# Kernel optimization log

Hardware: AMD Instinct MI355X
Metric: run time of the kernel (lower is better)

The kernel has to match this reference:

```python
import jax, jax.numpy as jnp
import numpy as np

B, S, D = 8, 2048, 64
NEG = -1e9


def setup_inputs() -> dict:
    key = jax.random.key(0)
    kq, kk, kv = jax.random.split(key, 3)
    return {
        "queries": jax.random.normal(kq, (B, S, D), dtype=jnp.float32),
        "keys": jax.random.normal(kk, (B, S, D), dtype=jnp.float32),
        "values": jax.random.normal(kv, (B, S, D), dtype=jnp.float32),
        "mask_q": jnp.ones((B, S), dtype=jnp.float32),
        "mask_k": jnp.ones((B, S), dtype=jnp.float32),
        "mask_v": jnp.ones((B, S), dtype=jnp.float32),
    }


def reference(queries, keys, values, mask_q, mask_k, mask_v):
    # scaled QK^T: [B, Sq, Sk]
    scaler = jnp.sqrt(jnp.asarray(queries.shape[-1], dtype=queries.dtype))
    scores = jnp.einsum("bqd,bkd->bqk", queries, keys) / scaler
    # additive padding mask from outer product of query/key masks
    padding_mask = mask_q[:, :, None] * mask_k[:, None, :]  # [B, Sq, Sk]
    scores = scores + (1.0 - padding_mask) * NEG
    attention_weights = jax.nn.softmax(scores, axis=-1)
    # mask values then weighted sum
    values = values * mask_v[:, :, None]
    output = jnp.einsum("bqk,bkd->bqd", attention_weights, values)
    return output
```

## Files before the change

kernel.cpp:

```cpp
#include <hip/hip_runtime.h>
#include <hip/hip_bf16.h>
#include <math.h>

#define BATCH 8
#define SEQ   2048
#define DIM   64
#define NEGC  (-1e9f)

typedef short short8  __attribute__((ext_vector_type(8)));
typedef float f32x4   __attribute__((ext_vector_type(4)));
typedef float f32x16  __attribute__((ext_vector_type(16)));

#define MFMA32(a, b, c) __builtin_amdgcn_mfma_f32_32x32x16_bf16((a), (b), (c), 0, 0, 0)

__device__ __forceinline__ ushort f2bf(float x) {
    uint u = __float_as_uint(x);
    uint r = (u + 0x7fffu + ((u >> 16) & 1u)) >> 16;
    return (ushort)r;
}
__device__ __forceinline__ float bf2f(ushort h) {
    return __uint_as_float(((uint)h) << 16);
}

__global__ __launch_bounds__(256)
void prep_kv(const float* __restrict__ K, const float* __restrict__ V,
             const float* __restrict__ MV, ushort* __restrict__ ws) {
    __shared__ float raw[64 * 68];
    const int t    = threadIdx.x;
    const int b    = blockIdx.x >> 5;
    const int tile = blockIdx.x & 31;
    const float* Kb  = K  + ((size_t)b * SEQ + tile * 64) * DIM;
    const float* Vb  = V  + ((size_t)b * SEQ + tile * 64) * DIM;
    const float* MVb = MV + (size_t)b * SEQ + tile * 64;
    ushort* wsI = ws + (size_t)(b * 32 + tile) * 8192;

#pragma unroll
    for (int u = 0; u < 4; u++) {
        int f = t + 256 * u, key = f >> 4, d4 = (f & 15) * 4;
        *(float4*)&raw[key * 68 + d4] = *(const float4*)(Kb + (size_t)f * 4);
    }
    __syncthreads();
#pragma unroll
    for (int u = 0; u < 2; u++) {
        int r = t + 256 * u;
        int mt = r >> 8, kc = (r >> 6) & 3, L = r & 63;
        int key = mt * 32 + (L & 31), d0 = kc * 16 + (L >> 5) * 8;
        float4 x0 = *(float4*)&raw[key * 68 + d0];
        float4 x1 = *(float4*)&raw[key * 68 + d0 + 4];
        float xs[8] = {x0.x, x0.y, x0.z, x0.w, x1.x, x1.y, x1.z, x1.w};
        short8 hv;
#pragma unroll
        for (int j = 0; j < 8; j++) hv[j] = (short)f2bf(xs[j]);
        *(short8*)(wsI + r * 8) = hv;
    }
    __syncthreads();

#pragma unroll
    for (int u = 0; u < 4; u++) {
        int f = t + 256 * u, key = f >> 4, d4 = (f & 15) * 4;
        float4 x = *(const float4*)(Vb + (size_t)f * 4);
        float mv = MVb[key];
        x.x *= mv; x.y *= mv; x.z *= mv; x.w *= mv;
        *(float4*)&raw[key * 68 + d4] = x;
    }
    __syncthreads();
#pragma unroll
    for (int u = 0; u < 2; u++) {
        int r = t + 256 * u;
        int dt = r >> 8, kc = (r >> 6) & 3, L = r & 63;
        int d = dt * 32 + (L & 31), k0 = kc * 16 + (L >> 5) * 8;
        short8 ov;
#pragma unroll
        for (int j = 0; j < 8; j++) ov[j] = (short)f2bf(raw[(k0 + j) * 68 + d]);
        *(short8*)(wsI + 4096 + r * 8) = ov;
    }
}

__global__ __launch_bounds__(512, 2)
void attn_fused(const float* __restrict__ Q, const float* __restrict__ MQ,
                const float* __restrict__ MK, const ushort* __restrict__ ws,
                float* __restrict__ O) {
    __shared__ __align__(16) float Msc[2][3][64][36];
    __shared__ __align__(16) float Oout[2][32][72];

    const int t    = threadIdx.x;
    const int w    = t >> 6;
    const int lane = t & 63;
    const int h    = lane >> 5;
    const int lm   = lane & 31;
    const int qg   = w & 1;
    const int ks   = w >> 1;

    const int b  = blockIdx.x & 7;
    const int qt = blockIdx.x >> 3;
    const int q  = qt * 64 + qg * 32 + lm;

    const float*  MKb = MK + (size_t)b * SEQ;
    const ushort* wsB = ws + (size_t)b * 32 * 8192;

    short8 qh[4], ql[4];
    {
        const float* Qr = Q + ((size_t)b * SEQ + q) * DIM;
#pragma unroll
        for (int kc = 0; kc < 4; kc++) {
            const float* p = Qr + kc * 16 + h * 8;
            float4 x0 = *(const float4*)p;
            float4 x1 = *(const float4*)(p + 4);
            float xs[8] = {x0.x, x0.y, x0.z, x0.w, x1.x, x1.y, x1.z, x1.w};
#pragma unroll
            for (int j = 0; j < 8; j++) {
                float v   = xs[j] * 0.125f;
                ushort hi = f2bf(v);
                ql[kc][j] = (short)f2bf(v - bf2f(hi));
                qh[kc][j] = (short)hi;
            }
        }
    }
    const float mq   = MQ[(size_t)b * SEQ + q];
    const float apen = NEGC * mq;

    float m = -1e30f, l = 0.0f;
    f32x16 ot0, ot1;
#pragma unroll
    for (int i = 0; i < 16; i++) { ot0[i] = 0.0f; ot1[i] = 0.0f; }

    auto loadch = [&](short8 (&kf)[4], short8 (&vf)[4], f32x4 (&bias)[4], int ch) {
        const int tt = ch >> 1, mt = ch & 1;
        const ushort* img = wsB + (size_t)tt * 8192;
#pragma unroll
        for (int kc = 0; kc < 4; kc++)
            kf[kc] = *(const short8*)(img + (((mt * 4 + kc) << 6) + lane) * 8);
#pragma unroll
        for (int u = 0; u < 4; u++) {
            const int dt = u >> 1, c = u & 1;
            vf[u] = *(const short8*)(img + 4096 + (((dt * 4 + mt * 2 + c) << 6) + lane) * 8);
        }
        const float* mkp = MKb + ch * 32 + h * 4;
#pragma unroll
        for (int v = 0; v < 4; v++) {
            f32x4 mk = *(const f32x4*)(mkp + v * 8);
#pragma unroll
            for (int c = 0; c < 4; c++) bias[v][c] = NEGC - apen * mk[c];
        }
    };

    auto step = [&](const short8 (&kf)[4], const short8 (&vf)[4],
                    const f32x4 (&bias)[4]) {
        f32x16 st;
#pragma unroll
        for (int i = 0; i < 16; i++) st[i] = 0.0f;
        __builtin_amdgcn_s_setprio(1);
#pragma unroll
        for (int kc = 0; kc < 4; kc++) {
            st = MFMA32(kf[kc], qh[kc], st);
            st = MFMA32(kf[kc], ql[kc], st);
        }
        __builtin_amdgcn_s_setprio(0);

        float sv[16];
#pragma unroll
        for (int v = 0; v < 4; v++)
#pragma unroll
            for (int c = 0; c < 4; c++)
                sv[v * 4 + c] = st[v * 4 + c] + bias[v][c];
        float cm = sv[0];
#pragma unroll
        for (int i = 1; i < 16; i++) cm = fmaxf(cm, sv[i]);
        cm = fmaxf(cm, __shfl_xor(cm, 32));
        if (!__all(cm <= m)) {
            float nm    = fmaxf(m, cm);
            float alpha = __expf(m - nm);
            m = nm;
            l *= alpha;
            ot0 *= alpha; ot1 *= alpha;
        }
        float p[16], cs = 0.0f;
#pragma unroll
        for (int i = 0; i < 16; i++) { p[i] = __expf(sv[i] - m); cs += p[i]; }
        cs += __shfl_xor(cs, 32);
        l += cs;

        uint g[4][2], x[4][2];
#pragma unroll
        for (int v = 0; v < 4; v++) {
            __hip_bfloat162 c0 = __float22bfloat162_rn(make_float2(p[v*4+0], p[v*4+1]));
            __hip_bfloat162 c1 = __float22bfloat162_rn(make_float2(p[v*4+2], p[v*4+3]));
            __builtin_memcpy(&g[v][0], &c0, 4);
            __builtin_memcpy(&g[v][1], &c1, 4);
            x[v][0] = (uint)__shfl_xor((int)g[v][0], 32);
            x[v][1] = (uint)__shfl_xor((int)g[v][1], 32);
        }
        uint pbw[2][4];
        pbw[0][0] = h ? x[1][0] : g[0][0];
        pbw[0][1] = h ? x[1][1] : g[0][1];
        pbw[0][2] = h ? g[1][0] : x[0][0];
        pbw[0][3] = h ? g[1][1] : x[0][1];
        pbw[1][0] = h ? x[3][0] : g[2][0];
        pbw[1][1] = h ? x[3][1] : g[2][1];
        pbw[1][2] = h ? g[3][0] : x[2][0];
        pbw[1][3] = h ? g[3][1] : x[2][1];

        __builtin_amdgcn_s_setprio(1);
#pragma unroll
        for (int c = 0; c < 2; c++) {
            short8 pb;
            __builtin_memcpy(&pb, &pbw[c][0], 16);
            ot0 = MFMA32(vf[c],     pb, ot0);
            ot1 = MFMA32(vf[2 + c], pb, ot1);
        }
        __builtin_amdgcn_s_setprio(0);
    };

    short8 kA[4], vA[4], kB[4], vB[4];
    f32x4  bA[4], bB[4];
    const int ch0 = ks * 16;
    loadch(kA, vA, bA, ch0);
#pragma unroll 1
    for (int i = 0; i < 8; i++) {
        loadch(kB, vB, bB, ch0 + 2 * i + 1);
        step(kA, vA, bA);
        if (i < 7) loadch(kA, vA, bA, ch0 + 2 * i + 2);
        step(kB, vB, bB);
    }

    if (ks != 0) {
        float* sc = &Msc[qg][ks - 1][lane][0];
#pragma unroll
        for (int i = 0; i < 4; i++) {
            f32x4 r0, r1;
#pragma unroll
            for (int c = 0; c < 4; c++) { r0[c] = ot0[i*4+c]; r1[c] = ot1[i*4+c]; }
            *(f32x4*)&sc[i * 4]      = r0;
            *(f32x4*)&sc[16 + i * 4] = r1;
        }
        sc[32] = m;
        sc[33] = l;
    }
    __syncthreads();
    if (ks == 0) {
#pragma unroll
        for (int pp = 0; pp < 3; pp++) {
            const float* sc = &Msc[qg][pp][lane][0];
            float mb = sc[32], lb = sc[33];
            float nm = fmaxf(m, mb);
            float fa = __expf(m - nm), fb = __expf(mb - nm);
            m = nm;
            l = l * fa + lb * fb;
#pragma unroll
            for (int i = 0; i < 16; i++) {
                ot0[i] = ot0[i] * fa + sc[i] * fb;
                ot1[i] = ot1[i] * fa + sc[16 + i] * fb;
            }
        }
        const float inv = 1.0f / l;
#pragma unroll
        for (int dt = 0; dt < 2; dt++)
#pragma unroll
            for (int rq = 0; rq < 4; rq++) {
                f32x4 r;
#pragma unroll
                for (int c = 0; c < 4; c++)
                    r[c] = (dt ? ot1[rq * 4 + c] : ot0[rq * 4 + c]) * inv;
                *(f32x4*)&Oout[qg][lm][dt * 32 + rq * 8 + h * 4] = r;
            }
    }
    __syncthreads();

    float* Ob = O + ((size_t)b * SEQ + qt * 64) * DIM;
#pragma unroll
    for (int u = 0; u < 2; u++) {
        int f = t + 512 * u;
        int row = f >> 4, d4 = (f & 15) * 4;
        f32x4 val = *(const f32x4*)&Oout[row >> 5][row & 31][d4];
        *(f32x4*)(Ob + (size_t)row * DIM + d4) = val;
    }
}

extern "C" void kernel_launch(void* const* d_in, const int* in_sizes, int n_in,
                              void* d_out, int out_size, void* d_ws, size_t ws_size,
                              hipStream_t stream) {
    const float* Q  = (const float*)d_in[0];
    const float* K  = (const float*)d_in[1];
    const float* V  = (const float*)d_in[2];
    const float* MQ = (const float*)d_in[3];
    const float* MK = (const float*)d_in[4];
    const float* MV = (const float*)d_in[5];
    float* O = (float*)d_out;

    ushort* wsKV = (ushort*)d_ws;

    prep_kv   <<<dim3(256), dim3(256), 0, stream>>>(K, V, MV, wsKV);
    attn_fused<<<dim3(256), dim3(512), 0, stream>>>(Q, MQ, MK, wsKV, O);
}
```

Measured before the change: 95.76 us.

## Use exp2 domain softmax, permlane32 swap, and split K/V prep blocks

Folds log2(e) into the query scale and mask bias so the softmax can use exp2 directly instead of exp. Replaces the shfl_xor-plus-select exchange of bf16 probabilities with permlane32_swap, and rebalances the max and sum reductions into shallower trees. Splits prep_kv so separate blocks handle K and V, doubling the grid to expose more parallelism. permlane32_swap is a gfx950-specific intrinsic, and its lane semantics must match the old select pattern.

```diff
diff --git a/kernel.cpp b/kernel.cpp
--- a/kernel.cpp
+++ b/kernel.cpp
@@ -5,11 +5,15 @@
 #define BATCH 8
 #define SEQ   2048
 #define DIM   64
-#define NEGC  (-1e9f)
+#define NEGC   (-1e9f)
+#define LOG2E  1.4426950408889634f
+#define QSC    (LOG2E / 8.0f)
+#define NEGC2  (-1.4426950408889634e9f)
 
 typedef short short8  __attribute__((ext_vector_type(8)));
 typedef float f32x4   __attribute__((ext_vector_type(4)));
 typedef float f32x16  __attribute__((ext_vector_type(16)));
+typedef unsigned int uint2v __attribute__((ext_vector_type(2)));
 
 #define MFMA32(a, b, c) __builtin_amdgcn_mfma_f32_32x32x16_bf16((a), (b), (c), 0, 0, 0)
 
@@ -27,52 +31,55 @@
              const float* __restrict__ MV, ushort* __restrict__ ws) {
     __shared__ float raw[64 * 68];
     const int t    = threadIdx.x;
-    const int b    = blockIdx.x >> 5;
-    const int tile = blockIdx.x & 31;
-    const float* Kb  = K  + ((size_t)b * SEQ + tile * 64) * DIM;
-    const float* Vb  = V  + ((size_t)b * SEQ + tile * 64) * DIM;
-    const float* MVb = MV + (size_t)b * SEQ + tile * 64;
+    const int b    = blockIdx.x & 7;
+    const int rr   = blockIdx.x >> 3;
+    const int tile = rr & 31;
+    const int kv   = rr >> 5;
     ushort* wsI = ws + (size_t)(b * 32 + tile) * 8192;
 
-#pragma unroll
-    for (int u = 0; u < 4; u++) {
-        int f = t + 256 * u, key = f >> 4, d4 = (f & 15) * 4;
-        *(float4*)&raw[key * 68 + d4] = *(const float4*)(Kb + (size_t)f * 4);
-    }
-    __syncthreads();
-#pragma unroll
-    for (int u = 0; u < 2; u++) {
-        int r = t + 256 * u;
-        int mt = r >> 8, kc = (r >> 6) & 3, L = r & 63;
-        int key = mt * 32 + (L & 31), d0 = kc * 16 + (L >> 5) * 8;
-        float4 x0 = *(float4*)&raw[key * 68 + d0];
-        float4 x1 = *(float4*)&raw[key * 68 + d0 + 4];
-        float xs[8] = {x0.x, x0.y, x0.z, x0.w, x1.x, x1.y, x1.z, x1.w};
-        short8 hv;
-#pragma unroll
-        for (int j = 0; j < 8; j++) hv[j] = (short)f2bf(xs[j]);
-        *(short8*)(wsI + r * 8) = hv;
-    }
-    __syncthreads();
-
-#pragma unroll
-    for (int u = 0; u < 4; u++) {
-        int f = t + 256 * u, key = f >> 4, d4 = (f & 15) * 4;
-        float4 x = *(const float4*)(Vb + (size_t)f * 4);
-        float mv = MVb[key];
-        x.x *= mv; x.y *= mv; x.z *= mv; x.w *= mv;
-        *(float4*)&raw[key * 68 + d4] = x;
-    }
-    __syncthreads();
-#pragma unroll
-    for (int u = 0; u < 2; u++) {
-        int r = t + 256 * u;
-        int dt = r >> 8, kc = (r >> 6) & 3, L = r & 63;
-        int d = dt * 32 + (L & 31), k0 = kc * 16 + (L >> 5) * 8;
-        short8 ov;
-#pragma unroll
-        for (int j = 0; j < 8; j++) ov[j] = (short)f2bf(raw[(k0 + j) * 68 + d]);
-        *(short8*)(wsI + 4096 + r * 8) = ov;
+    if (kv == 0) {
+        const float* Kb = K + ((size_t)b * SEQ + tile * 64) * DIM;
+#pragma unroll
+        for (int u = 0; u < 4; u++) {
+            int f = t + 256 * u, key = f >> 4, d4 = (f & 15) * 4;
+            *(float4*)&raw[key * 68 + d4] = *(const float4*)(Kb + (size_t)f * 4);
+        }
+        __syncthreads();
+#pragma unroll
+        for (int u = 0; u < 2; u++) {
+            int r = t + 256 * u;
+            int mt = r >> 8, kc = (r >> 6) & 3, L = r & 63;
+            int key = mt * 32 + (L & 31), d0 = kc * 16 + (L >> 5) * 8;
+            float4 x0 = *(float4*)&raw[key * 68 + d0];
+            float4 x1 = *(float4*)&raw[key * 68 + d0 + 4];
+            float xs[8] = {x0.x, x0.y, x0.z, x0.w, x1.x, x1.y, x1.z, x1.w};
+            short8 hv;
+#pragma unroll
+            for (int j = 0; j < 8; j++) hv[j] = (short)f2bf(xs[j]);
+            *(short8*)(wsI + r * 8) = hv;
+        }
+    } else {
+        const float* Vb  = V  + ((size_t)b * SEQ + tile * 64) * DIM;
+        const float* MVb = MV + (size_t)b * SEQ + tile * 64;
+#pragma unroll
+        for (int u = 0; u < 4; u++) {
+            int f = t + 256 * u, key = f >> 4, d4 = (f & 15) * 4;
+            float4 x = *(const float4*)(Vb + (size_t)f * 4);
+            float mv = MVb[key];
+            x.x *= mv; x.y *= mv; x.z *= mv; x.w *= mv;
+            *(float4*)&raw[key * 68 + d4] = x;
+        }
+        __syncthreads();
+#pragma unroll
+        for (int u = 0; u < 2; u++) {
+            int r = t + 256 * u;
+            int dt = r >> 8, kc = (r >> 6) & 3, L = r & 63;
+            int d = dt * 32 + (L & 31), k0 = kc * 16 + (L >> 5) * 8;
+            short8 ov;
+#pragma unroll
+            for (int j = 0; j < 8; j++) ov[j] = (short)f2bf(raw[(k0 + j) * 68 + d]);
+            *(short8*)(wsI + 4096 + r * 8) = ov;
+        }
     }
 }
 
@@ -109,15 +116,15 @@
             float xs[8] = {x0.x, x0.y, x0.z, x0.w, x1.x, x1.y, x1.z, x1.w};
 #pragma unroll
             for (int j = 0; j < 8; j++) {
-                float v   = xs[j] * 0.125f;
+                float v   = xs[j] * QSC;
                 ushort hi = f2bf(v);
                 ql[kc][j] = (short)f2bf(v - bf2f(hi));
                 qh[kc][j] = (short)hi;
             }
         }
     }
-    const float mq   = MQ[(size_t)b * SEQ + q];
-    const float apen = NEGC * mq;
+    const float mq    = MQ[(size_t)b * SEQ + q];
+    const float apen2 = NEGC2 * mq;
 
     float m = -1e30f, l = 0.0f;
     f32x16 ot0, ot1;
@@ -140,7 +147,7 @@
         for (int v = 0; v < 4; v++) {
             f32x4 mk = *(const f32x4*)(mkp + v * 8);
 #pragma unroll
-            for (int c = 0; c < 4; c++) bias[v][c] = NEGC - apen * mk[c];
+            for (int c = 0; c < 4; c++) bias[v][c] = NEGC2 - apen2 * mk[c];
         }
     };
 
@@ -163,42 +170,46 @@
 #pragma unroll
             for (int c = 0; c < 4; c++)
                 sv[v * 4 + c] = st[v * 4 + c] + bias[v][c];
-        float cm = sv[0];
-#pragma unroll
-        for (int i = 1; i < 16; i++) cm = fmaxf(cm, sv[i]);
+        float t0 = fmaxf(fmaxf(sv[0],  sv[1]),  sv[2]);
+        float t1 = fmaxf(fmaxf(sv[3],  sv[4]),  sv[5]);
+        float t2 = fmaxf(fmaxf(sv[6],  sv[7]),  sv[8]);
+        float t3 = fmaxf(fmaxf(sv[9],  sv[10]), sv[11]);
+        float t4 = fmaxf(fmaxf(sv[12], sv[13]), sv[14]);
+        float cm = fmaxf(fmaxf(fmaxf(t0, t1), t2),
+                         fmaxf(fmaxf(t3, t4), sv[15]));
         cm = fmaxf(cm, __shfl_xor(cm, 32));
         if (!__all(cm <= m)) {
             float nm    = fmaxf(m, cm);
-            float alpha = __expf(m - nm);
+            float alpha = exp2f(m - nm);
             m = nm;
             l *= alpha;
             ot0 *= alpha; ot1 *= alpha;
         }
-        float p[16], cs = 0.0f;
-#pragma unroll
-        for (int i = 0; i < 16; i++) { p[i] = __expf(sv[i] - m); cs += p[i]; }
+        float p[16];
+#pragma unroll
+        for (int i = 0; i < 16; i++) p[i] = exp2f(sv[i] - m);
+        float s0 = (p[0] + p[1]) + (p[2] + p[3]);
+        float s1 = (p[4] + p[5]) + (p[6] + p[7]);
+        float s2 = (p[8] + p[9]) + (p[10] + p[11]);
+        float s3 = (p[12] + p[13]) + (p[14] + p[15]);
+        float cs = (s0 + s1) + (s2 + s3);
         cs += __shfl_xor(cs, 32);
         l += cs;
 
-        uint g[4][2], x[4][2];
+        uint g[4][2];
 #pragma unroll
         for (int v = 0; v < 4; v++) {
             __hip_bfloat162 c0 = __float22bfloat162_rn(make_float2(p[v*4+0], p[v*4+1]));
             __hip_bfloat162 c1 = __float22bfloat162_rn(make_float2(p[v*4+2], p[v*4+3]));
             __builtin_memcpy(&g[v][0], &c0, 4);
             __builtin_memcpy(&g[v][1], &c1, 4);
-            x[v][0] = (uint)__shfl_xor((int)g[v][0], 32);
-            x[v][1] = (uint)__shfl_xor((int)g[v][1], 32);
-        }
-        uint pbw[2][4];
-        pbw[0][0] = h ? x[1][0] : g[0][0];
-        pbw[0][1] = h ? x[1][1] : g[0][1];
-        pbw[0][2] = h ? g[1][0] : x[0][0];
-        pbw[0][3] = h ? g[1][1] : x[0][1];
-        pbw[1][0] = h ? x[3][0] : g[2][0];
-        pbw[1][1] = h ? x[3][1] : g[2][1];
-        pbw[1][2] = h ? g[3][0] : x[2][0];
-        pbw[1][3] = h ? g[3][1] : x[2][1];
+        }
+        uint2v ra = __builtin_amdgcn_permlane32_swap(g[0][0], g[1][0], false, false);
+        uint2v rb = __builtin_amdgcn_permlane32_swap(g[0][1], g[1][1], false, false);
+        uint2v rc = __builtin_amdgcn_permlane32_swap(g[2][0], g[3][0], false, false);
+        uint2v rd = __builtin_amdgcn_permlane32_swap(g[2][1], g[3][1], false, false);
+        uint pbw[2][4] = {{ra[0], rb[0], ra[1], rb[1]},
+                          {rc[0], rd[0], rc[1], rd[1]}};
 
         __builtin_amdgcn_s_setprio(1);
 #pragma unroll
@@ -243,7 +254,7 @@
             const float* sc = &Msc[qg][pp][lane][0];
             float mb = sc[32], lb = sc[33];
             float nm = fmaxf(m, mb);
-            float fa = __expf(m - nm), fb = __expf(mb - nm);
+            float fa = exp2f(m - nm), fb = exp2f(mb - nm);
             m = nm;
             l = l * fa + lb * fb;
 #pragma unroll
@@ -289,6 +300,6 @@
 
     ushort* wsKV = (ushort*)d_ws;
 
-    prep_kv   <<<dim3(256), dim3(256), 0, stream>>>(K, V, MV, wsKV);
+    prep_kv   <<<dim3(512), dim3(256), 0, stream>>>(K, V, MV, wsKV);
     attn_fused<<<dim3(256), dim3(512), 0, stream>>>(Q, MQ, MK, wsKV, O);
 }
```

Result: slower. 99.97 us (+4.4%).
